# Optimization experiments

Hardware: AMD Instinct MI355X
Metric: run time of the kernel (lower is better)

The kernel has to match this reference:

```python
import jax, jax.numpy as jnp
import numpy as np

NUM_MELS = 80
FPS = 2            # frames_per_step
ENC = 512
ATT = 512          # attention_rnn_dim
DEC = 512          # decoder_rnn_dim
PRE = 256          # prenet_dims[-1]
M = 5              # num_mixtures
Q_HID = 256        # MoL query MLP hidden
B = 16
T_ENC = 600
T_MEL = 1200


def setup_inputs() -> dict:
    key = jax.random.key(0)
    ks = jax.random.split(key, 16)
    g = lambda k, shape: (jax.random.normal(k, shape, dtype=jnp.float32) * 0.05)
    f32 = jnp.float32
    inp = {
        'memory': jax.random.normal(ks[0], (B, T_ENC, ENC), f32),
        'mel_inputs': jax.random.normal(ks[1], (B, T_MEL, NUM_MELS), f32),
        'memory_lengths': jax.random.randint(ks[2], (B,), 1, T_ENC + 1),
        'memory_pitch': jax.random.normal(ks[3], (B, T_ENC, ENC), f32),
        # prenet (bias-free linears)
        'prenet_w1': g(ks[4], (PRE, NUM_MELS)),
        'prenet_w2': g(ks[5], (PRE, PRE)),
        # attention LSTMCell: input = prenet_out + context = PRE + ENC
        'att_wih': g(ks[6], (4 * ATT, PRE + ENC)),
        'att_whh': g(ks[7], (4 * ATT, ATT)),
        'att_bih': jnp.zeros((4 * ATT,), f32),
        'att_bhh': jnp.zeros((4 * ATT,), f32),
        # MoL attention query MLP: Linear(ATT,256)-tanh-Linear(256,3M)
        'q_w1': g(ks[8], (Q_HID, ATT)),
        'q_b1': jnp.zeros((Q_HID,), f32),
        'q_w2': g(ks[9], (3 * M, Q_HID)),
        # bias init: sigma part = 1.0, Delta part = 0.5413 (softplus -> ~1)
        'q_b2': jnp.concatenate([jnp.zeros((M,), f32), jnp.ones((M,), f32), jnp.full((M,), 0.5413, f32)]),
        # decoder LSTMCell: input = att_h + ctx + ctx_pitch = ATT + 2*ENC
        'dec_wih': g(ks[10], (4 * DEC, 2 * ENC + ATT)),
        'dec_whh': g(ks[11], (4 * DEC, DEC)),
        'dec_bih': jnp.zeros((4 * DEC,), f32),
        'dec_bhh': jnp.zeros((4 * DEC,), f32),
        # projection: (dec_h, ctx, ctx_pitch) -> num_mels*fps
        'proj_w': g(ks[12], (NUM_MELS * FPS, 2 * ENC + DEC)),
        'proj_b': jnp.zeros((NUM_MELS * FPS,), f32),
    }
    return inp


def _lstm_cell(x, h, c, wih, whh, bih, bhh):
    gates = x @ wih.T + bih + h @ whh.T + bhh
    i, f, g, o = jnp.split(gates, 4, axis=-1)
    c2 = jax.nn.sigmoid(f) * c + jax.nn.sigmoid(i) * jnp.tanh(g)
    h2 = jax.nn.sigmoid(o) * jnp.tanh(c2)
    return h2, c2


def _forward(memory, mel_inputs, memory_lengths, memory_pitch,
             prenet_w1, prenet_w2, att_wih, att_whh, att_bih, att_bhh,
             q_w1, q_b1, q_w2, q_b2, dec_wih, dec_whh, dec_bih, dec_bhh,
             proj_w, proj_b):
    Bv, T_enc, enc_dim = memory.shape
    T_dec = mel_inputs.shape[1] // FPS

    # parse_decoder_inputs: (B,T_mel,nmels) -> (T_dec,B,nmels), keep last frame of each group
    dec_in = mel_inputs.reshape(Bv, T_dec, -1)[:, :, -NUM_MELS:]
    dec_in = jnp.transpose(dec_in, (1, 0, 2))
    go = jnp.zeros((1, Bv, NUM_MELS), mel_inputs.dtype)
    dec_in = jnp.concatenate([go, dec_in], axis=0)  # (T_dec+1,B,nmels)

    # prenet: relu->dropout(0.5, always on)->relu->dropout; fixed-seed masks for determinism
    dk1, dk2 = jax.random.split(jax.random.key(42))
    x = jax.nn.relu(dec_in @ prenet_w1.T)
    x = jnp.where(jax.random.bernoulli(dk1, 0.5, x.shape), x * 2.0, 0.0)
    x = jax.nn.relu(x @ prenet_w2.T)
    x = jnp.where(jax.random.bernoulli(dk2, 0.5, x.shape), x * 2.0, 0.0)
    prenet_out = x[:T_dec]  # only steps 0..T_dec-1 are consumed by the loop

    # padding mask (True where padded) and MoL positions j = arange + 0.5
    mask_pad = jnp.arange(T_enc)[None, :] >= memory_lengths[:, None]  # (B,T_enc)
    j = jnp.arange(T_enc, dtype=memory.dtype)[None, None, :] + 0.5  # (1,1,T_enc)

    def step(carry, pn):
        att_h, att_c, dec_h, dec_c, ctx, mu_prev = carry
        # attention RNN
        cell_in = jnp.concatenate([pn, ctx], axis=-1)
        att_h, att_c = _lstm_cell(cell_in, att_h, att_c, att_wih, att_whh, att_bih, att_bhh)
        # MoL mixture params
        q = jnp.tanh(att_h @ q_w1.T + q_b1) @ q_w2.T + q_b2  # (B,3M)
        w = jax.nn.softmax(q[:, :M], axis=-1) + 1e-6
        sigma = jax.nn.softplus(q[:, M:2 * M]) + 0.5
        delta = jax.nn.softplus(q[:, 2 * M:])
        mu = mu_prev + delta  # (B,M), monotone forward movement
        # logistic CDF differences -> alignment
        zc = (j - mu[:, :, None]) / sigma[:, :, None]  # (B,M,T_enc), centered
        h = 0.5 / sigma[:, :, None]
        alpha = jnp.sum(w[:, :, None] * (jax.nn.sigmoid(zc + h) - jax.nn.sigmoid(zc - h)), axis=1)  # (B,T_enc)
        alpha = jnp.where(mask_pad, 0.0, alpha)
        ctx = jnp.einsum('bt,btd->bd', alpha, memory)
        ctx_p = jnp.einsum('bt,btd->bd', alpha, memory_pitch)
        # decoder RNN + projection (concat_context_to_last=True)
        dec_h, dec_c = _lstm_cell(jnp.concatenate([att_h, ctx, ctx_p], axis=-1), dec_h, dec_c,
                                  dec_wih, dec_whh, dec_bih, dec_bhh)
        out = jnp.concatenate([dec_h, ctx, ctx_p], axis=-1)
        mel = out @ proj_w.T + proj_b  # (B, nmels*fps)
        return (att_h, att_c, dec_h, dec_c, ctx, mu), (mel, alpha)

    z = lambda d: jnp.zeros((Bv, d), memory.dtype)
    carry0 = (z(ATT), z(ATT), z(DEC), z(DEC), z(enc_dim), jnp.zeros((Bv, M), memory.dtype))
    _, (mels, alphas) = jax.lax.scan(step, carry0, prenet_out)

    mel_outputs = jnp.transpose(mels, (1, 0, 2)).reshape(Bv, -1, NUM_MELS)  # (B,T_mel,nmels)
    alignments = jnp.transpose(alphas, (1, 0, 2))  # (B,T_dec,T_enc)
    return mel_outputs, alignments


def reference(memory, mel_inputs, memory_lengths, memory_pitch,
              prenet_w1, prenet_w2, att_wih, att_whh, att_bih, att_bhh,
              q_w1, q_b1, q_w2, q_b2, dec_wih, dec_whh, dec_bih, dec_bhh,
              proj_w, proj_b):
    return _forward(memory, mel_inputs, memory_lengths, memory_pitch,
                    prenet_w1, prenet_w2, att_wih, att_whh, att_bih, att_bhh,
                    q_w1, q_b1, q_w2, q_b2, dec_wih, dec_whh, dec_bih, dec_bhh,
                    proj_w, proj_b)
```

## Files before the change

### kernel.cpp

```cpp
#include <hip/hip_runtime.h>

#define NB_SCAN   240
#define NT_SCAN   512
#define TDEC      600
#define ALIGN_OFF 1536000

#define NGRP  16
#define GRPSZ 15

#define WS_ATT_H     0
#define WS_ATT_C     16384
#define WS_DEC_H     24576
#define WS_DEC_C     40960
#define WS_CTX       49152
#define WS_CTXP      65536
#define WS_STATE_END 82176
#define WS_PN        131072

struct BarSt {
  unsigned grp[NGRP][128];
  unsigned root[128];
  unsigned gen;
  unsigned pad[31];
};
__device__ BarSt barst;

__device__ __forceinline__ void bar_arrive(int g, unsigned k, int tid){
  __syncthreads();
  if (tid == 0) {
    unsigned* gs = &barst.grp[g][(k & 3u)*32];
    unsigned r = __hip_atomic_fetch_add(gs, 1u, __ATOMIC_ACQ_REL, __HIP_MEMORY_SCOPE_AGENT);
    if (r == GRPSZ-1u) {
      __hip_atomic_store(gs, 0u, __ATOMIC_RELAXED, __HIP_MEMORY_SCOPE_AGENT);
      unsigned* rs = &barst.root[(k & 3u)*32];
      unsigned rr = __hip_atomic_fetch_add(rs, 1u, __ATOMIC_ACQ_REL, __HIP_MEMORY_SCOPE_AGENT);
      if (rr == NGRP-1u) {
        __hip_atomic_store(rs, 0u, __ATOMIC_RELAXED, __HIP_MEMORY_SCOPE_AGENT);
        __hip_atomic_store(&barst.gen, k + 1u, __ATOMIC_RELEASE, __HIP_MEMORY_SCOPE_AGENT);
      }
    }
  }
}

__device__ __forceinline__ void bar_wait(unsigned k, int tid){
  if (tid == 0) {
    const unsigned tgt = k + 1u;
    while ((int)(__hip_atomic_load(&barst.gen, __ATOMIC_RELAXED, __HIP_MEMORY_SCOPE_AGENT) - tgt) < 0)
      __builtin_amdgcn_s_sleep(1);
    (void)__hip_atomic_load(&barst.gen, __ATOMIC_ACQUIRE, __HIP_MEMORY_SCOPE_AGENT);
  }
  __syncthreads();
}

__host__ __device__ inline unsigned rotl_(unsigned x, int n){ return (x<<n)|(x>>(32-n)); }
__host__ __device__ inline void threefry2x32(unsigned k0, unsigned k1,
                                             unsigned x0, unsigned x1,
                                             unsigned &o0, unsigned &o1){
  unsigned ks[3] = {k0, k1, k0 ^ k1 ^ 0x1BD11BDAu};
  x0 += ks[0]; x1 += ks[1];
  const int R0[4] = {13,15,26,6};
  const int R1[4] = {17,29,16,24};
  #pragma unroll
  for (int i = 0; i < 5; ++i) {
    const int* R = (i & 1) ? R1 : R0;
    #pragma unroll
    for (int j = 0; j < 4; ++j) { x0 += x1; x1 = rotl_(x1, R[j]); x1 ^= x0; }
    x0 += ks[(i+1)%3];
    x1 += ks[(i+2)%3] + (unsigned)(i+1);
  }
  o0 = x0; o1 = x1;
}

__device__ __forceinline__ bool keep_mask(unsigned i, unsigned k0, unsigned k1){
  unsigned o0, o1;
  threefry2x32(k0, k1, 0u, i, o0, o1);
  return (((o0 ^ o1) >> 31) == 0u);
}

__device__ __forceinline__ float sigm_(float x){ return 1.f / (1.f + expf(-x)); }
__device__ __forceinline__ float softplus_(float x){ return log1pf(expf(-fabsf(x))) + fmaxf(x, 0.f); }

__device__ __forceinline__ void dot4(float& acc, const float* __restrict__ w,
                                     const float* __restrict__ x, int n){
  const float4* __restrict__ w4 = (const float4*)w;
  const float4* __restrict__ x4 = (const float4*)x;
  const int n4 = n >> 2;
  #pragma unroll 8
  for (int k = 0; k < n4; ++k) {
    float4 a = w4[k], v = x4[k];
    acc = fmaf(a.x, v.x, acc); acc = fmaf(a.y, v.y, acc);
    acc = fmaf(a.z, v.z, acc); acc = fmaf(a.w, v.w, acc);
  }
}

#define RSTAGE(v, lane, h, cnt) { const bool hi_ = ((lane) & (h)) != 0;      \
  _Pragma("unroll") for (int i_ = 0; i_ < (cnt); ++i_) {                     \
    float s_ = hi_ ? (v)[i_] : (v)[i_+(cnt)];                                \
    float k_ = hi_ ? (v)[i_+(cnt)] : (v)[i_];                                \
    (v)[i_] = k_ + __shfl_xor(s_, (h), 64); } }

__global__ __launch_bounds__(256) void prenet_kernel(
    const float* __restrict__ mel, const float* __restrict__ w1,
    const float* __restrict__ w2, float* __restrict__ ws,
    unsigned k1a, unsigned k1b, unsigned k2a, unsigned k2b)
{
  __shared__ float in_s[16][84];
  __shared__ float x1_s[16][260];
  const int t = blockIdx.x;
  const int tid = threadIdx.x;

  if (t == 0) {
    unsigned* p = (unsigned*)&barst;
    for (int i = tid; i < (int)(sizeof(BarSt)/4); i += 256) p[i] = 0u;
  }

  for (int i = tid; i < 16*80; i += 256) {
    int b = i / 80, c = i - b*80;
    float v = 0.f;
    if (t > 0) v = mel[((size_t)b*1200 + (2*t-1))*80 + c];
    in_s[b][c] = v;
  }
  __syncthreads();

  const int j2 = tid >> 4, b = tid & 15;

  for (int jo = 0; jo < 16; ++jo) {
    int j = jo*16 + j2;
    float acc = 0.f;
    dot4(acc, w1 + (size_t)j*80, &in_s[b][0], 80);
    acc = fmaxf(acc, 0.f);
    unsigned idx = ((unsigned)t*16u + (unsigned)b)*256u + (unsigned)j;
    acc = keep_mask(idx, k1a, k1b) ? acc*2.f : 0.f;
    x1_s[b][j] = acc;
  }
  __syncthreads();

  for (int jo = 0; jo < 16; ++jo) {
    int j = jo*16 + j2;
    float acc = 0.f;
    dot4(acc, w2 + (size_t)j*256, &x1_s[b][0], 256);
    acc = fmaxf(acc, 0.f);
    unsigned idx = ((unsigned)t*16u + (unsigned)b)*256u + (unsigned)j;
    acc = keep_mask(idx, k2a, k2b) ? acc*2.f : 0.f;
    ws[WS_PN + ((size_t)t*16 + b)*256 + j] = acc;
  }
}

struct ScanArgs {
  const float* memory; const float* memory_pitch; const int* mlen;
  const float* att_wih; const float* att_whh; const float* att_bih; const float* att_bhh;
  const float* q_w1; const float* q_b1; const float* q_w2; const float* q_b2;
  const float* dec_wih; const float* dec_whh; const float* dec_bih; const float* dec_bhh;
  const float* proj_w; const float* proj_b;
  float* out; float* ws;
};

union ShMem {
  struct { float xs[8][1280]; } att;
  struct { float xs[4][2048]; float dbuf[4][64]; } dec;
  struct { float ah[512]; float q1s[256]; float q2s[16];
           float sc[20]; float alpha[600]; float mun[8];
           int iv[4]; } q;
};

__device__ __forceinline__ void att_role(const ScanArgs& A, ShMem& sh,
                                         int blk, int tid, int g)
{
  float* ws = A.ws;
  float* attH = ws + WS_ATT_H; float* attC = ws + WS_ATT_C;
  float* ctxB = ws + WS_CTX;
  const float* pn = ws + WS_PN;
  const int lane = tid & 63, wv = tid >> 6;
  const int unit = blk*8 + wv;

  float4 w4[4][5];
  #pragma unroll
  for (int gate = 0; gate < 4; ++gate) {
    int row = gate*512 + unit;
    #pragma unroll
    for (int c = 0; c < 5; ++c) {
      int k = c*256 + lane*4;
      const float* s = (k < 768) ? A.att_wih + (size_t)row*768 + k
                                 : A.att_whh + (size_t)row*512 + (k - 768);
      w4[gate][c] = *(const float4*)s;
    }
  }
  const int brow = (lane >> 4)*512 + unit;
  const float bias = A.att_bih[brow] + A.att_bhh[brow];

  unsigned k = 1;
  for (int t = 0; t <= TDEC; ++t, k += 2) {
    const int pc = t & 1, pp = (t + 1) & 1;
    if (t < TDEC) {
      float acc[64];
      #pragma unroll
      for (int i = 0; i < 64; ++i) acc[i] = 0.f;
      #pragma unroll
      for (int bc = 0; bc < 2; ++bc) {
        __syncthreads();
        for (int i = tid; i < 8*320; i += NT_SCAN) {
          int b8 = i / 320, k4 = i - b8*320, kk = k4*4, b = bc*8 + b8;
          float4 v;
          if (kk < 256)      v = *(const float4*)(pn + ((size_t)t*16 + b)*256 + kk);
          else if (kk < 768) v = *(const float4*)(ctxB + pp*8192 + b*512 + (kk-256));
          else               v = *(const float4*)(attH + pp*8192 + b*512 + (kk-768));
          *(float4*)&sh.att.xs[b8][kk] = v;
        }
        __syncthreads();
        #pragma unroll
        for (int b8 = 0; b8 < 8; ++b8) {
          float4 x4[5];
          #pragma unroll
          for (int c = 0; c < 5; ++c) x4[c] = *(const float4*)&sh.att.xs[b8][c*256 + lane*4];
          #pragma unroll
          for (int gate = 0; gate < 4; ++gate) {
            float s = acc[gate*16 + bc*8 + b8];
            #pragma unroll
            for (int c = 0; c < 5; ++c) {
              s = fmaf(w4[gate][c].x, x4[c].x, s); s = fmaf(w4[gate][c].y, x4[c].y, s);
              s = fmaf(w4[gate][c].z, x4[c].z, s); s = fmaf(w4[gate][c].w, x4[c].w, s);
            }
            acc[gate*16 + bc*8 + b8] = s;
          }
        }
      }
      RSTAGE(acc, lane, 32, 32) RSTAGE(acc, lane, 16, 16) RSTAGE(acc, lane, 8, 8)
      RSTAGE(acc, lane, 4, 4)   RSTAGE(acc, lane, 2, 2)   RSTAGE(acc, lane, 1, 1)
      float g0 = acc[0] + bias;
      float gf = __shfl(g0, 16 + (lane & 15), 64);
      float gg = __shfl(g0, 32 + (lane & 15), 64);
      float go = __shfl(g0, 48 + (lane & 15), 64);
      if (lane < 16) {
        int b = lane;
        float c  = attC[b*512 + unit];
        float c2 = sigm_(gf)*c + sigm_(g0)*tanhf(gg);
        float h2 = sigm_(go)*tanhf(c2);
        attC[b*512 + unit] = c2;
        attH[pc*8192 + b*512 + unit] = h2;
      }
    }
    bar_arrive(g, k, tid);
    bar_arrive(g, k+1, tid);
    bar_wait(k+1, tid);
  }
}

__device__ __forceinline__ void dec_role(const ScanArgs& A, ShMem& sh,
                                         int blk, int tid, int g)
{
  float* ws = A.ws;
  float* attH = ws + WS_ATT_H; float* decH = ws + WS_DEC_H; float* decC = ws + WS_DEC_C;
  float* ctxB = ws + WS_CTX;   float* ctpB = ws + WS_CTXP;
  const int lane = tid & 63, wv = tid >> 6;
  const int db = blk - 64;
  const int unit = db*4 + (wv & 3);
  const int half = wv >> 2, ul = wv & 3;

  float4 w4[4][4];
  #pragma unroll
  for (int gate = 0; gate < 4; ++gate) {
    int row = gate*512 + unit;
    #pragma unroll
    for (int c = 0; c < 4; ++c) {
      int k = half*1024 + c*256 + lane*4;
      const float* s = (k < 1536) ? A.dec_wih + (size_t)row*1536 + k
                                  : A.dec_whh + (size_t)row*512 + (k - 1536);
      w4[gate][c] = *(const float4*)s;
    }
  }
  const int brow = (lane >> 4)*512 + unit;
  const float bias = A.dec_bih[brow] + A.dec_bhh[brow];

  unsigned k = 1;
  for (int t = 0; t <= TDEC; ++t, k += 2) {
    const int pc = t & 1, pp = (t + 1) & 1;
    if (t >= 1) {
      float acc[64];
      #pragma unroll
      for (int i = 0; i < 64; ++i) acc[i] = 0.f;
      #pragma unroll
      for (int bc = 0; bc < 4; ++bc) {
        __syncthreads();
        for (int i = tid; i < 4*512; i += NT_SCAN) {
          int b4 = i >> 9, k4 = i & 511, kk = k4*4, b = bc*4 + b4;
          float4 v;
          if (kk < 512)       v = *(const float4*)(attH + pp*8192 + b*512 + kk);
          else if (kk < 1024) v = *(const float4*)(ctxB + pp*8192 + b*512 + (kk-512));
          else if (kk < 1536) v = *(const float4*)(ctpB + pp*8192 + b*512 + (kk-1024));
          else                v = *(const float4*)(decH + pc*8192 + b*512 + (kk-1536));
          *(float4*)&sh.dec.xs[b4][kk] = v;
        }
        __syncthreads();
        #pragma unroll
        for (int b4 = 0; b4 < 4; ++b4) {
          float4 x4[4];
          #pragma unroll
          for (int c = 0; c < 4; ++c) x4[c] = *(const float4*)&sh.dec.xs[b4][half*1024 + c*256 + lane*4];
          #pragma unroll
          for (int gate = 0; gate < 4; ++gate) {
            float s = acc[gate*16 + bc*4 + b4];
            #pragma unroll
            for (int c = 0; c < 4; ++c) {
              s = fmaf(w4[gate][c].x, x4[c].x, s); s = fmaf(w4[gate][c].y, x4[c].y, s);
              s = fmaf(w4[gate][c].z, x4[c].z, s); s = fmaf(w4[gate][c].w, x4[c].w, s);
            }
            acc[gate*16 + bc*4 + b4] = s;
          }
        }
      }
      RSTAGE(acc, lane, 32, 32) RSTAGE(acc, lane, 16, 16) RSTAGE(acc, lane, 8, 8)
      RSTAGE(acc, lane, 4, 4)   RSTAGE(acc, lane, 2, 2)   RSTAGE(acc, lane, 1, 1)
      if (half == 1) sh.dec.dbuf[ul][lane] = acc[0];
      __syncthreads();
      float g0 = acc[0] + sh.dec.dbuf[ul][lane] + bias;
      float gf = __shfl(g0, 16 + (lane & 15), 64);
      float gg = __shfl(g0, 32 + (lane & 15), 64);
      float go = __shfl(g0, 48 + (lane & 15), 64);
      if (half == 0 && lane < 16) {
        int b = lane;
        float c  = decC[b*512 + unit];
        float c2 = sigm_(gf)*c + sigm_(g0)*tanhf(gg);
        float h2 = sigm_(go)*tanhf(c2);
        decC[b*512 + unit] = c2;
        decH[pp*8192 + b*512 + unit] = h2;
      }
    }
    bar_arrive(g, k, tid);
    bar_arrive(g, k+1, tid);
    bar_wait(k+1, tid);
  }
}

__device__ __forceinline__ void q_role(const ScanArgs& A, ShMem& sh,
                                       int blk, int tid, int g)
{
  float* ws = A.ws;
  float* attH = ws + WS_ATT_H;
  float* ctxB = ws + WS_CTX; float* ctpB = ws + WS_CTXP;
  const int qi = blk - 192, b = qi >> 1, half = qi & 1;
  const int mlen_b = A.mlen[b];

  if (tid < 8) sh.q.mun[tid] = 0.f;

  unsigned k = 1;
  for (int t = 0; t <= TDEC; ++t, k += 2) {
    const int pc = t & 1;
    bar_arrive(g, k, tid);
    bar_wait(k, tid);
    if (t < TDEC) {
      sh.q.ah[tid] = attH[pc*8192 + b*512 + tid];
      __syncthreads();
      {
        const int row = tid >> 1, kq = tid & 1;
        const float4* wr = (const float4*)(A.q_w1 + (size_t)row*512 + kq*256);
        const float4* xr = (const float4*)&sh.q.ah[kq*256];
        float s0 = 0.f, s1 = 0.f;
        #pragma unroll 8
        for (int j = 0; j < 32; ++j) {
          float4 a = wr[2*j],   v = xr[2*j];
          s0 = fmaf(a.x, v.x, s0); s0 = fmaf(a.y, v.y, s0);
          s0 = fmaf(a.z, v.z, s0); s0 = fmaf(a.w, v.w, s0);
          float4 a2 = wr[2*j+1], v2 = xr[2*j+1];
          s1 = fmaf(a2.x, v2.x, s1); s1 = fmaf(a2.y, v2.y, s1);
          s1 = fmaf(a2.z, v2.z, s1); s1 = fmaf(a2.w, v2.w, s1);
        }
        float s = s0 + s1;
        s += __shfl_xor(s, 1, 64);
        if (kq == 0) sh.q.q1s[row] = tanhf(s + A.q_b1[row]);
      }
      __syncthreads();
      if (tid < 240) {
        const int row = tid >> 4, l16 = tid & 15;
        const float4* wr = (const float4*)(A.q_w2 + (size_t)row*256 + l16*16);
        const float4* xr = (const float4*)&sh.q.q1s[l16*16];
        float s = 0.f;
        #pragma unroll
        for (int j = 0; j < 4; ++j) {
          float4 a = wr[j], v = xr[j];
          s = fmaf(a.x, v.x, s); s = fmaf(a.y, v.y, s);
          s = fmaf(a.z, v.z, s); s = fmaf(a.w, v.w, s);
        }
        s += __shfl_xor(s, 1, 64); s += __shfl_xor(s, 2, 64);
        s += __shfl_xor(s, 4, 64); s += __shfl_xor(s, 8, 64);
        if (l16 == 0) sh.q.q2s[row] = s + A.q_b2[row];
      }
      __syncthreads();
      if (tid == 0) {
        float mx = -1e30f;
        for (int m = 0; m < 5; ++m) mx = fmaxf(mx, sh.q.q2s[m]);
        float ssum = 0.f, e[5];
        for (int m = 0; m < 5; ++m) { e[m] = expf(sh.q.q2s[m]-mx); ssum += e[m]; }
        float mn = 1e30f, mxu = -1e30f;
        for (int m = 0; m < 5; ++m) {
          float wv2 = e[m]/ssum + 1e-6f;
          float sg  = softplus_(sh.q.q2s[5+m]) + 0.5f;
          float is  = 1.f/sg;
          float dl  = softplus_(sh.q.q2s[10+m]);
          float mu  = sh.q.mun[m] + dl;
          sh.q.sc[m] = wv2; sh.q.sc[5+m] = is; sh.q.sc[10+m] = 0.5f*is; sh.q.sc[15+m] = mu;
          sh.q.mun[m] = mu;
          mn = fminf(mn, mu); mxu = fmaxf(mxu, mu);
        }
        int lo = (int)floorf(mn) - 56; if (lo < 0) lo = 0;
        int hi = (int)ceilf(mxu) + 57; if (hi > TDEC) hi = TDEC;
        sh.q.iv[0] = lo; sh.q.iv[1] = hi;
      }
      __syncthreads();
      const int lo = sh.q.iv[0], hi = sh.q.iv[1];
      for (int te = tid; te < TDEC; te += NT_SCAN) {
        float a = 0.f;
        if (te >= lo && te < hi && te < mlen_b) {
          float jj = te + 0.5f;
          #pragma unroll
          for (int m = 0; m < 5; ++m) {
            float zc = (jj - sh.q.sc[15+m]) * sh.q.sc[5+m];
            float hh = sh.q.sc[10+m];
            a += sh.q.sc[m] * (sigm_(zc+hh) - sigm_(zc-hh));
          }
        }
        sh.q.alpha[te] = a;
        if (half == 0)
          A.out[ALIGN_OFF + (size_t)b*360000 + (size_t)t*600 + te] = a;
      }
      __syncthreads();
      {
        const float* mem = half ? A.memory_pitch : A.memory;
        float a0=0.f, a1=0.f, a2=0.f, a3=0.f;
        int te = lo;
        for (; te + 3 < hi; te += 4) {
          const float* mp = mem + ((size_t)b*600 + te)*512 + tid;
          a0 = fmaf(sh.q.alpha[te],   mp[0],    a0);
          a1 = fmaf(sh.q.alpha[te+1], mp[512],  a1);
          a2 = fmaf(sh.q.alpha[te+2], mp[1024], a2);
          a3 = fmaf(sh.q.alpha[te+3], mp[1536], a3);
        }
        for (; te < hi; ++te)
          a0 = fmaf(sh.q.alpha[te], mem[((size_t)b*600 + te)*512 + tid], a0);
        (half ? ctpB : ctxB)[pc*8192 + b*512 + tid] = (a0+a1)+(a2+a3);
      }
    }
    bar_arrive(g, k+1, tid);
  }
}

__device__ __forceinline__ void proj_role(const ScanArgs& A, ShMem& sh,
                                          int blk, int tid, int g)
{
  float* ws = A.ws;
  float* decH = ws + WS_DEC_H; float* ctxB = ws + WS_CTX; float* ctpB = ws + WS_CTXP;
  const int lane = tid & 63;
  const bool act = (tid < 320);
  const int row = (blk-224)*10 + (tid >> 5);
  const int l32 = tid & 31;

  float4 w4[12]; float pb = 0.f;
  if (act) {
    #pragma unroll
    for (int c = 0; c < 12; ++c)
      w4[c] = *(const float4*)(A.proj_w + (size_t)row*1536 + c*128 + l32*4);
    pb = A.proj_b[row];
  }

  unsigned k = 1;
  for (int t = 0; t <= TDEC; ++t, k += 2) {
    const int pp = (t + 1) & 1;
    bar_arrive(g, k, tid);
    bar_wait(k, tid);
    if (t >= 1 && act) {
      float acc[16];
      #pragma unroll
      for (int i = 0; i < 16; ++i) acc[i] = 0.f;
      #pragma unroll
      for (int b = 0; b < 16; ++b) {
        #pragma unroll
        for (int c = 0; c < 12; ++c) {
          int kk = c*128 + l32*4;
          const float* xp = (kk < 512) ? decH + pp*8192 + b*512 + kk
                          : (kk < 1024) ? ctxB + pp*8192 + b*512 + (kk-512)
                                        : ctpB + pp*8192 + b*512 + (kk-1024);
          float4 v = *(const float4*)xp;
          float s = acc[b];
          s = fmaf(w4[c].x, v.x, s); s = fmaf(w4[c].y, v.y, s);
          s = fmaf(w4[c].z, v.z, s); s = fmaf(w4[c].w, v.w, s);
          acc[b] = s;
        }
      }
      #pragma unroll
      for (int i = 0; i < 16; ++i) acc[i] += __shfl_xor(acc[i], 16, 64);
      RSTAGE(acc, lane, 8, 8) RSTAGE(acc, lane, 4, 4)
      RSTAGE(acc, lane, 2, 2) RSTAGE(acc, lane, 1, 1)
      if ((lane & 31) < 16) {
        int b = lane & 15;
        A.out[(size_t)b*96000 + (size_t)(t-1)*160 + row] = acc[0] + pb;
      }
    }
    bar_arrive(g, k+1, tid);
  }
}

__global__ __launch_bounds__(NT_SCAN) void scan_kernel(ScanArgs A)
{
  const int blk = blockIdx.x, tid = threadIdx.x;
  const int g = blk / GRPSZ;
  __shared__ ShMem sh;

  for (int i = blk*NT_SCAN + tid; i < WS_STATE_END; i += NB_SCAN*NT_SCAN) A.ws[i] = 0.f;

  bar_arrive(g, 0, tid);
  bar_wait(0, tid);

  if (blk < 64)       att_role(A, sh, blk, tid, g);
  else if (blk < 192) dec_role(A, sh, blk, tid, g);
  else if (blk < 224) q_role(A, sh, blk, tid, g);
  else                proj_role(A, sh, blk, tid, g);
}

extern "C" void kernel_launch(void* const* d_in, const int* in_sizes, int n_in,
                              void* d_out, int out_size, void* d_ws, size_t ws_size,
                              hipStream_t stream) {
  const float* memory = (const float*)d_in[0];
  const float* mel    = (const float*)d_in[1];
  const int*   mlen   = (const int*)  d_in[2];
  const float* memp   = (const float*)d_in[3];
  const float* pw1    = (const float*)d_in[4];
  const float* pw2    = (const float*)d_in[5];

  ScanArgs args;
  args.memory = memory; args.memory_pitch = memp; args.mlen = mlen;
  args.att_wih = (const float*)d_in[6];  args.att_whh = (const float*)d_in[7];
  args.att_bih = (const float*)d_in[8];  args.att_bhh = (const float*)d_in[9];
  args.q_w1    = (const float*)d_in[10]; args.q_b1    = (const float*)d_in[11];
  args.q_w2    = (const float*)d_in[12]; args.q_b2    = (const float*)d_in[13];
  args.dec_wih = (const float*)d_in[14]; args.dec_whh = (const float*)d_in[15];
  args.dec_bih = (const float*)d_in[16]; args.dec_bhh = (const float*)d_in[17];
  args.proj_w  = (const float*)d_in[18]; args.proj_b  = (const float*)d_in[19];
  args.out = (float*)d_out; args.ws = (float*)d_ws;

  unsigned dk1a, dk1b, dk2a, dk2b;
  threefry2x32(0u, 42u, 0u, 0u, dk1a, dk1b);
  threefry2x32(0u, 42u, 0u, 1u, dk2a, dk2b);

  prenet_kernel<<<dim3(600), dim3(256), 0, stream>>>(mel, pw1, pw2, (float*)d_ws,
                                                     dk1a, dk1b, dk2a, dk2b);

  void* kp[] = { &args };
  hipLaunchCooperativeKernel((void*)scan_kernel, dim3(NB_SCAN), dim3(NT_SCAN),
                             kp, 0, stream);
}
```

Baseline: 33.16 ms.

## Replace global tree barriers with per-block progress flags and quad buffering

Drops the hierarchical grid-wide barrier in favour of a per-block monotonic progress flag array. Each role waits only on the flags of the roles whose outputs it reads, at step-specific targets. State buffers go from double to quadruple buffering, so roles can run several steps out of phase without overwriting data still being read. This is meant to remove lockstep barrier latency and let the attention, query, decoder and projection stages pipeline across timesteps. In exchange, every block polls up to 240 flags per step, and correctness now depends on the flag offsets matching the buffer reuse distances.

```diff
diff --git a/kernel.cpp b/kernel.cpp
--- a/kernel.cpp
+++ b/kernel.cpp
@@ -5,50 +5,37 @@
 #define TDEC      600
 #define ALIGN_OFF 1536000
 
-#define NGRP  16
-#define GRPSZ 15
-
 #define WS_ATT_H     0
-#define WS_ATT_C     16384
-#define WS_DEC_H     24576
-#define WS_DEC_C     40960
-#define WS_CTX       49152
-#define WS_CTXP      65536
-#define WS_STATE_END 82176
-#define WS_PN        131072
-
-struct BarSt {
-  unsigned grp[NGRP][128];
-  unsigned root[128];
-  unsigned gen;
-  unsigned pad[31];
-};
-__device__ BarSt barst;
-
-__device__ __forceinline__ void bar_arrive(int g, unsigned k, int tid){
+#define WS_ATT_C     32768
+#define WS_DEC_H     40960
+#define WS_DEC_C     73728
+#define WS_CTX       81920
+#define WS_CTXP      114688
+#define WS_STATE_END 147456
+#define WS_PN        163840
+
+__device__ unsigned Fdev[256];
+
+__device__ __forceinline__ void post_flag(int blk, unsigned val, int tid){
   __syncthreads();
-  if (tid == 0) {
-    unsigned* gs = &barst.grp[g][(k & 3u)*32];
-    unsigned r = __hip_atomic_fetch_add(gs, 1u, __ATOMIC_ACQ_REL, __HIP_MEMORY_SCOPE_AGENT);
-    if (r == GRPSZ-1u) {
-      __hip_atomic_store(gs, 0u, __ATOMIC_RELAXED, __HIP_MEMORY_SCOPE_AGENT);
-      unsigned* rs = &barst.root[(k & 3u)*32];
-      unsigned rr = __hip_atomic_fetch_add(rs, 1u, __ATOMIC_ACQ_REL, __HIP_MEMORY_SCOPE_AGENT);
-      if (rr == NGRP-1u) {
-        __hip_atomic_store(rs, 0u, __ATOMIC_RELAXED, __HIP_MEMORY_SCOPE_AGENT);
-        __hip_atomic_store(&barst.gen, k + 1u, __ATOMIC_RELEASE, __HIP_MEMORY_SCOPE_AGENT);
-      }
-    }
-  }
-}
-
-__device__ __forceinline__ void bar_wait(unsigned k, int tid){
-  if (tid == 0) {
-    const unsigned tgt = k + 1u;
-    while ((int)(__hip_atomic_load(&barst.gen, __ATOMIC_RELAXED, __HIP_MEMORY_SCOPE_AGENT) - tgt) < 0)
+  if (tid == 0)
+    __hip_atomic_store(&Fdev[blk], val, __ATOMIC_RELEASE, __HIP_MEMORY_SCOPE_AGENT);
+}
+
+__device__ __forceinline__ void wait_flags(int tid, int ta, int td, int tq, int tp){
+  int tgt;
+  if (tid < 64) tgt = ta;
+  else if (tid < 192) tgt = td;
+  else if (tid < 224) tgt = tq;
+  else if (tid < 240) tgt = tp;
+  else tgt = 0;
+  if (tgt > 0) {
+    while ((int)__hip_atomic_load(&Fdev[tid], __ATOMIC_RELAXED, __HIP_MEMORY_SCOPE_AGENT) < tgt)
       __builtin_amdgcn_s_sleep(1);
-    (void)__hip_atomic_load(&barst.gen, __ATOMIC_ACQUIRE, __HIP_MEMORY_SCOPE_AGENT);
-  }
+  }
+  __syncthreads();
+  if (tid == 0)
+    (void)__hip_atomic_load(&Fdev[0], __ATOMIC_ACQUIRE, __HIP_MEMORY_SCOPE_AGENT);
   __syncthreads();
 }
 
@@ -109,10 +96,7 @@
   const int t = blockIdx.x;
   const int tid = threadIdx.x;
 
-  if (t == 0) {
-    unsigned* p = (unsigned*)&barst;
-    for (int i = tid; i < (int)(sizeof(BarSt)/4); i += 256) p[i] = 0u;
-  }
+  if (t == 0 && tid < 256) Fdev[tid] = 0u;
 
   for (int i = tid; i < 16*80; i += 256) {
     int b = i / 80, c = i - b*80;
@@ -164,7 +148,7 @@
 };
 
 __device__ __forceinline__ void att_role(const ScanArgs& A, ShMem& sh,
-                                         int blk, int tid, int g)
+                                         int blk, int tid)
 {
   float* ws = A.ws;
   float* attH = ws + WS_ATT_H; float* attC = ws + WS_ATT_C;
@@ -188,10 +172,10 @@
   const int brow = (lane >> 4)*512 + unit;
   const float bias = A.att_bih[brow] + A.att_bhh[brow];
 
-  unsigned k = 1;
-  for (int t = 0; t <= TDEC; ++t, k += 2) {
-    const int pc = t & 1, pp = (t + 1) & 1;
-    if (t < TDEC) {
+  for (int t = 0; t < TDEC; ++t) {
+    const int pc = t & 3, pr = (t + 3) & 3;
+    wait_flags(tid, 0, t-1, t+1, 0);
+    {
       float acc[64];
       #pragma unroll
       for (int i = 0; i < 64; ++i) acc[i] = 0.f;
@@ -202,8 +186,8 @@
           int b8 = i / 320, k4 = i - b8*320, kk = k4*4, b = bc*8 + b8;
           float4 v;
           if (kk < 256)      v = *(const float4*)(pn + ((size_t)t*16 + b)*256 + kk);
-          else if (kk < 768) v = *(const float4*)(ctxB + pp*8192 + b*512 + (kk-256));
-          else               v = *(const float4*)(attH + pp*8192 + b*512 + (kk-768));
+          else if (kk < 768) v = *(const float4*)(ctxB + pr*8192 + b*512 + (kk-256));
+          else               v = *(const float4*)(attH + pr*8192 + b*512 + (kk-768));
           *(float4*)&sh.att.xs[b8][kk] = v;
         }
         __syncthreads();
@@ -239,14 +223,12 @@
         attH[pc*8192 + b*512 + unit] = h2;
       }
     }
-    bar_arrive(g, k, tid);
-    bar_arrive(g, k+1, tid);
-    bar_wait(k+1, tid);
+    post_flag(blk, t+2, tid);
   }
 }
 
 __device__ __forceinline__ void dec_role(const ScanArgs& A, ShMem& sh,
-                                         int blk, int tid, int g)
+                                         int blk, int tid)
 {
   float* ws = A.ws;
   float* attH = ws + WS_ATT_H; float* decH = ws + WS_DEC_H; float* decC = ws + WS_DEC_C;
@@ -271,9 +253,9 @@
   const int brow = (lane >> 4)*512 + unit;
   const float bias = A.dec_bih[brow] + A.dec_bhh[brow];
 
-  unsigned k = 1;
-  for (int t = 0; t <= TDEC; ++t, k += 2) {
-    const int pc = t & 1, pp = (t + 1) & 1;
+  for (int t = 0; t <= TDEC; ++t) {
+    const int pr = (t + 3) & 3, pd2 = (t + 2) & 3;
+    wait_flags(tid, 0, t+1, t+1, t-2);
     if (t >= 1) {
       float acc[64];
       #pragma unroll
@@ -284,10 +266,10 @@
         for (int i = tid; i < 4*512; i += NT_SCAN) {
           int b4 = i >> 9, k4 = i & 511, kk = k4*4, b = bc*4 + b4;
           float4 v;
-          if (kk < 512)       v = *(const float4*)(attH + pp*8192 + b*512 + kk);
-          else if (kk < 1024) v = *(const float4*)(ctxB + pp*8192 + b*512 + (kk-512));
-          else if (kk < 1536) v = *(const float4*)(ctpB + pp*8192 + b*512 + (kk-1024));
-          else                v = *(const float4*)(decH + pc*8192 + b*512 + (kk-1536));
+          if (kk < 512)       v = *(const float4*)(attH + pr*8192 + b*512 + kk);
+          else if (kk < 1024) v = *(const float4*)(ctxB + pr*8192 + b*512 + (kk-512));
+          else if (kk < 1536) v = *(const float4*)(ctpB + pr*8192 + b*512 + (kk-1024));
+          else                v = *(const float4*)(decH + pd2*8192 + b*512 + (kk-1536));
           *(float4*)&sh.dec.xs[b4][kk] = v;
         }
         __syncthreads();
@@ -322,17 +304,15 @@
         float c2 = sigm_(gf)*c + sigm_(g0)*tanhf(gg);
         float h2 = sigm_(go)*tanhf(c2);
         decC[b*512 + unit] = c2;
-        decH[pp*8192 + b*512 + unit] = h2;
+        decH[pr*8192 + b*512 + unit] = h2;
       }
     }
-    bar_arrive(g, k, tid);
-    bar_arrive(g, k+1, tid);
-    bar_wait(k+1, tid);
+    post_flag(blk, t+2, tid);
   }
 }
 
 __device__ __forceinline__ void q_role(const ScanArgs& A, ShMem& sh,
-                                       int blk, int tid, int g)
+                                       int blk, int tid)
 {
   float* ws = A.ws;
   float* attH = ws + WS_ATT_H;
@@ -342,12 +322,10 @@
 
   if (tid < 8) sh.q.mun[tid] = 0.f;
 
-  unsigned k = 1;
-  for (int t = 0; t <= TDEC; ++t, k += 2) {
-    const int pc = t & 1;
-    bar_arrive(g, k, tid);
-    bar_wait(k, tid);
-    if (t < TDEC) {
+  for (int t = 0; t < TDEC; ++t) {
+    const int pc = t & 3;
+    wait_flags(tid, t+2, t-1, 0, t-1);
+    {
       sh.q.ah[tid] = attH[pc*8192 + b*512 + tid];
       __syncthreads();
       {
@@ -439,12 +417,12 @@
         (half ? ctpB : ctxB)[pc*8192 + b*512 + tid] = (a0+a1)+(a2+a3);
       }
     }
-    bar_arrive(g, k+1, tid);
+    post_flag(blk, t+2, tid);
   }
 }
 
 __device__ __forceinline__ void proj_role(const ScanArgs& A, ShMem& sh,
-                                          int blk, int tid, int g)
+                                          int blk, int tid)
 {
   float* ws = A.ws;
   float* decH = ws + WS_DEC_H; float* ctxB = ws + WS_CTX; float* ctpB = ws + WS_CTXP;
@@ -461,11 +439,9 @@
     pb = A.proj_b[row];
   }
 
-  unsigned k = 1;
-  for (int t = 0; t <= TDEC; ++t, k += 2) {
-    const int pp = (t + 1) & 1;
-    bar_arrive(g, k, tid);
-    bar_wait(k, tid);
+  for (int t = 0; t <= TDEC; ++t) {
+    const int pr = (t + 3) & 3;
+    wait_flags(tid, 0, t+2, t+1, 0);
     if (t >= 1 && act) {
       float acc[16];
       #pragma unroll
@@ -475,9 +451,9 @@
         #pragma unroll
         for (int c = 0; c < 12; ++c) {
           int kk = c*128 + l32*4;
-          const float* xp = (kk < 512) ? decH + pp*8192 + b*512 + kk
-                          : (kk < 1024) ? ctxB + pp*8192 + b*512 + (kk-512)
-                                        : ctpB + pp*8192 + b*512 + (kk-1024);
+          const float* xp = (kk < 512) ? decH + pr*8192 + b*512 + kk
+                          : (kk < 1024) ? ctxB + pr*8192 + b*512 + (kk-512)
+                                        : ctpB + pr*8192 + b*512 + (kk-1024);
           float4 v = *(const float4*)xp;
           float s = acc[b];
           s = fmaf(w4[c].x, v.x, s); s = fmaf(w4[c].y, v.y, s);
@@ -494,25 +470,24 @@
         A.out[(size_t)b*96000 + (size_t)(t-1)*160 + row] = acc[0] + pb;
       }
     }
-    bar_arrive(g, k+1, tid);
+    post_flag(blk, t+2, tid);
   }
 }
 
 __global__ __launch_bounds__(NT_SCAN) void scan_kernel(ScanArgs A)
 {
   const int blk = blockIdx.x, tid = threadIdx.x;
-  const int g = blk / GRPSZ;
   __shared__ ShMem sh;
 
   for (int i = blk*NT_SCAN + tid; i < WS_STATE_END; i += NB_SCAN*NT_SCAN) A.ws[i] = 0.f;
 
-  bar_arrive(g, 0, tid);
-  bar_wait(0, tid);
-
-  if (blk < 64)       att_role(A, sh, blk, tid, g);
-  else if (blk < 192) dec_role(A, sh, blk, tid, g);
-  else if (blk < 224) q_role(A, sh, blk, tid, g);
-  else                proj_role(A, sh, blk, tid, g);
+  post_flag(blk, 1, tid);
+  wait_flags(tid, 1, 1, 1, 1);
+
+  if (blk < 64)       att_role(A, sh, blk, tid);
+  else if (blk < 192) dec_role(A, sh, blk, tid);
+  else if (blk < 224) q_role(A, sh, blk, tid);
+  else                proj_role(A, sh, blk, tid);
 }
 
 extern "C" void kernel_launch(void* const* d_in, const int* in_sizes, int n_in,
```

After: 31.44 ms. 1.05x faster.
